# Kernel tuning notes

Hardware: AMD Instinct MI355X
Metric: run time of the kernel (lower is better)

## Reference

```python
import jax, jax.numpy as jnp
import numpy as np

EPS = 1e-5
NEG = 0.1  # LeakyReLU slope


def _conv(x, w, stride=1, pad=0):
    return jax.lax.conv_general_dilated(
        x, w, (stride, stride), [(pad, pad), (pad, pad)],
        dimension_numbers=('NCHW', 'OIHW', 'NCHW'))


def _bn(x, p):
    # p: [4, C] stacked (gamma, beta, running_mean, running_var); eval-mode BN
    g, b, m, v = p[0], p[1], p[2], p[3]
    inv = g / jnp.sqrt(v + EPS)
    return x * inv[None, :, None, None] + (b - m * inv)[None, :, None, None]


def _lrelu(x):
    return jnp.where(x >= 0, x, NEG * x)


def _mdcn(x, w_off, b_off, w_dcn, b_dcn, G=2, K=3, pad=1):
    # ModulatedDeformConvPack (DCNv2): conv_offset -> (dy, dx, mask), then
    # modulated bilinear sampling + dense contraction with the conv weight.
    B, C, H, W = x.shape
    K2 = K * K
    off = _conv(x, w_off, 1, pad) + b_off[None, :, None, None]  # [B, 3*G*K2, H, W]
    dy, dx, ml = jnp.split(off, 3, axis=1)
    dy = dy.reshape(B, G, K2, H, W)
    dx = dx.reshape(B, G, K2, H, W)
    mask = jax.nn.sigmoid(ml).reshape(B, G, K2, H, W)
    kyv, kxv = np.meshgrid(np.arange(K), np.arange(K), indexing='ij')
    ky = jnp.asarray(kyv.reshape(K2), x.dtype)
    kx = jnp.asarray(kxv.reshape(K2), x.dtype)
    ii = jnp.arange(H, dtype=x.dtype)
    jj = jnp.arange(W, dtype=x.dtype)
    # sample coords: p0 + p_k + offset (stride 1, dilation 1)
    py = ii[None, None, None, :, None] - pad + ky[None, None, :, None, None] + dy
    px = jj[None, None, None, None, :] - pad + kx[None, None, :, None, None] + dx
    Cg = C // G
    # [B, G, H*W, Cg] layout so the bilinear gather indexes a small int tensor
    imgs = x.reshape(B, G, Cg, H, W).transpose(0, 1, 3, 4, 2).reshape(B, G, H * W, Cg)
    y0 = jnp.floor(py)
    x0 = jnp.floor(px)
    N = K2 * H * W
    wy = (py - y0).reshape(B, G, N, 1)
    wx = (px - x0).reshape(B, G, N, 1)

    def gather(yi, xi):
        valid = (yi >= 0) & (yi <= H - 1) & (xi >= 0) & (xi <= W - 1)
        yc = jnp.clip(yi, 0, H - 1).astype(jnp.int32)
        xc = jnp.clip(xi, 0, W - 1).astype(jnp.int32)
        idx = (yc * W + xc).reshape(B, G, N, 1)
        v = jnp.take_along_axis(imgs, idx, axis=2)  # [B, G, N, Cg]
        return v * valid.reshape(B, G, N, 1).astype(x.dtype)

    v00 = gather(y0, x0)
    v01 = gather(y0, x0 + 1)
    v10 = gather(y0 + 1, x0)
    v11 = gather(y0 + 1, x0 + 1)
    val = (v00 * (1 - wy) * (1 - wx) + v01 * (1 - wy) * wx
           + v10 * wy * (1 - wx) + v11 * wy * wx)
    val = (val * mask.reshape(B, G, N, 1)).reshape(B, G, K2, H, W, Cg)
    wr = w_dcn.reshape(w_dcn.shape[0], G, Cg, K2)
    out = jnp.einsum('bgkijc,ogck->boij', val, wr)
    return out + b_dcn[None, :, None, None]


def _forward(x, w_r1, bn_r1, w_r2, bn_r2, w_rs, bn_rs, w_off, b_off,
             w_dcn, b_dcn, bn1, w_c2, bn2, w_ds, bn_ds):
    # ResBlock(in=64, out=128, stride=2): conv3x3/s2-BN-LReLU-conv3x3-BN + 1x1/s2 shortcut
    h = _lrelu(_bn(_conv(x, w_r1, 2, 1), bn_r1))
    h = _bn(_conv(h, w_r2, 1, 1), bn_r2)
    sc = _bn(_conv(x, w_rs, 2, 0), bn_rs)
    h = _lrelu(h + sc)
    # modulated deformable conv 3x3, deformable_groups=2
    h = _lrelu(_bn(_mdcn(h, w_off, b_off, w_dcn, b_dcn), bn1))
    h = _lrelu(_bn(_conv(h, w_c2, 1, 0), bn2))
    # DeconBlock residual (downsample since in!=out, stride!=1)
    res = _bn(_conv(x, w_ds, 2, 0), bn_ds)
    return res + h


def setup_inputs() -> dict:
    key = jax.random.key(0)
    ks = jax.random.split(key, 16)
    f32 = jnp.float32

    def n(k, shape, s):
        return jax.random.normal(k, shape, f32) * s

    def bnp(k, c):
        # gamma, beta, mean, var — var kept >= 0.1 for stability
        return jax.random.uniform(k, (4, c), f32, 0.1, 1.0)

    return {
        'x': n(ks[0], (4, 64, 192, 192), 1.0),
        'w_r1': n(ks[1], (128, 64, 3, 3), 0.04),
        'bn_r1': bnp(ks[2], 128),
        'w_r2': n(ks[3], (128, 128, 3, 3), 0.03),
        'bn_r2': bnp(ks[4], 128),
        'w_rs': n(ks[5], (128, 64, 1, 1), 0.12),
        'bn_rs': bnp(ks[6], 128),
        'w_off': n(ks[7], (54, 128, 3, 3), 0.01),  # small => offsets of a few px
        'b_off': n(ks[8], (54,), 0.1),
        'w_dcn': n(ks[9], (128, 128, 3, 3), 0.03),
        'b_dcn': n(ks[10], (128,), 0.1),
        'bn1': bnp(ks[11], 128),
        'w_c2': n(ks[12], (128, 128, 1, 1), 0.09),
        'bn2': bnp(ks[13], 128),
        'w_ds': n(ks[14], (128, 64, 1, 1), 0.12),
        'bn_ds': bnp(ks[15], 128),
    }


def reference(x, w_r1, bn_r1, w_r2, bn_r2, w_rs, bn_rs, w_off, b_off,
              w_dcn, b_dcn, bn1, w_c2, bn2, w_ds, bn_ds):
    return _forward(x, w_r1, bn_r1, w_r2, bn_r2, w_rs, bn_rs, w_off, b_off,
                    w_dcn, b_dcn, bn1, w_c2, bn2, w_ds, bn_ds)
```

## Files before the change

kernel.cpp:

```cpp
#include <hip/hip_runtime.h>
#include <hip/hip_bf16.h>
#include <cstdint>

#define EPS 1e-5f
#define NEG 0.1f

using bfrag = __attribute__((ext_vector_type(8))) short;
using f32x4 = __attribute__((ext_vector_type(4))) float;
typedef unsigned short ushort_t;

constexpr int B_  = 4,  CIN = 64, H0 = 192, W0 = 192;
constexpr int C_  = 128, H_ = 96, W_ = 96;
constexpr int HW_ = H_ * W_;
constexpr int HW0 = H0 * W0;
constexpr int XS  = 194;
constexpr int TS  = 98;
constexpr int VSTR = 1160;

__device__ __forceinline__ ushort_t f2bf(float f) {
  unsigned u = __builtin_bit_cast(unsigned, f);
  u += 0x7fffu + ((u >> 16) & 1u);
  return (ushort_t)(u >> 16);
}
__device__ __forceinline__ float loF(unsigned d) {
  return __builtin_bit_cast(float, d << 16);
}
__device__ __forceinline__ float hiF(unsigned d) {
  return __builtin_bit_cast(float, d & 0xFFFF0000u);
}
__device__ __forceinline__ bfrag loadB(const ushort_t* p) {
  return *(const bfrag*)p;
}

#define MFMA4(A0, A1, B0, B1, ACC)                                             \
  ACC[0][0] = __builtin_amdgcn_mfma_f32_16x16x32_bf16(A0, B0, ACC[0][0], 0, 0, 0); \
  ACC[0][1] = __builtin_amdgcn_mfma_f32_16x16x32_bf16(A0, B1, ACC[0][1], 0, 0, 0); \
  ACC[1][0] = __builtin_amdgcn_mfma_f32_16x16x32_bf16(A1, B0, ACC[1][0], 0, 0, 0); \
  ACC[1][1] = __builtin_amdgcn_mfma_f32_16x16x32_bf16(A1, B1, ACC[1][1], 0, 0, 0);

__global__ __launch_bounds__(256)
void k_prep(const float* __restrict__ x,
            const float* __restrict__ w_r1, const float* __restrict__ w_r2,
            const float* __restrict__ w_off, const float* __restrict__ w_dcn,
            const float* __restrict__ w_rs, const float* __restrict__ w_c2,
            const float* __restrict__ w_ds,
            ushort_t* __restrict__ wp_r1, ushort_t* __restrict__ wp_r2,
            ushort_t* __restrict__ wp_off, ushort_t* __restrict__ wp_dcn,
            ushort_t* __restrict__ wp_rs, ushort_t* __restrict__ wp_c2,
            ushort_t* __restrict__ wp_ds,
            ushort_t* __restrict__ xclp, ushort_t* __restrict__ t1p,
            ushort_t* __restrict__ t3p) {
  __shared__ float tile[64][65];
  int bi = blockIdx.x;
  int tid = (int)threadIdx.x;
  auto pack3w = [&](const float* w, ushort_t* wp, int O, int C, int Opad, int b0) {
    int idx = (bi - b0) * 256 + tid;
    int e = idx & 7;
    int lane = (idx >> 3) & 63;
    int fb = idx >> 9;
    int OBQ = Opad / 16;
    int obq = fb % OBQ, s = fb / OBQ;
    int lr = lane & 15, lq = lane >> 4;
    int o = obq * 16 + lr;
    int cq = s % (C / 32), tap = s / (C / 32);
    int c = cq * 32 + lq * 8 + e;
    wp[idx] = (o < O) ? f2bf(w[((size_t)o * C + c) * 9 + tap]) : (ushort_t)0;
  };
  auto pack1w = [&](const float* w, ushort_t* wp, int O, int C, int Opad, int b0) {
    int idx = (bi - b0) * 256 + tid;
    int e = idx & 7;
    int lane = (idx >> 3) & 63;
    int fb = idx >> 9;
    int OBQ = Opad / 16;
    int obq = fb % OBQ, s = fb / OBQ;
    int lr = lane & 15, lq = lane >> 4;
    int o = obq * 16 + lr;
    int c = s * 32 + lq * 8 + e;
    wp[idx] = (o < O) ? f2bf(w[(size_t)o * C + c]) : (ushort_t)0;
  };
  auto border = [&](ushort_t* buf, int N, int C, int b0) {
    int idx = (bi - b0) * 256 + tid;
    int per = 4 * N - 4;
    if (idx >= per * 4) return;
    int b = idx / per, e = idx - b * per;
    int r, s;
    if (e < N) { r = 0; s = e; }
    else if (e < 2 * N) { r = N - 1; s = e - N; }
    else if (e < 3 * N - 2) { r = e - 2 * N + 1; s = 0; }
    else { r = e - (3 * N - 2) + 1; s = N - 1; }
    uint4* p = (uint4*)(buf + ((size_t)(b * N + r) * N + s) * C);
#pragma unroll
    for (int t = 0; t < 16; ++t) { if (t < C / 8) p[t] = make_uint4(0, 0, 0, 0); }
  };
  if      (bi <  288) pack3w(w_r1,  wp_r1, 128,  64, 128, 0);
  else if (bi <  864) pack3w(w_r2,  wp_r2, 128, 128, 128, 288);
  else if (bi < 1152) pack3w(w_off, wp_off, 54, 128,  64, 864);
  else if (bi < 1728) pack3w(w_dcn, wp_dcn, 128, 128, 128, 1152);
  else if (bi < 1760) pack1w(w_rs,  wp_rs, 128,  64, 128, 1728);
  else if (bi < 1824) pack1w(w_c2,  wp_c2, 128, 128, 128, 1760);
  else if (bi < 1856) pack1w(w_ds,  wp_ds, 128,  64, 128, 1824);
  else if (bi < 1869) border(xclp, XS, 64, 1856);
  else if (bi < 1876) border(t1p, TS, 128, 1869);
  else if (bi < 1883) border(t3p, TS, 128, 1876);
  else {
    int bx = bi - 1883;
    int cx = bx % 3;
    int rem = bx / 3;
    int y = rem % 192, b = rem / 192;
    int tx = tid & 63, ty = tid >> 6;
    const float* src = x + (size_t)b * CIN * HW0 + (size_t)y * W0 + cx * 64;
#pragma unroll
    for (int r = 0; r < 16; ++r) {
      int ch = r * 4 + ty;
      tile[ch][tx] = src[(size_t)ch * HW0 + tx];
    }
    __syncthreads();
    ushort_t* dst = xclp + ((size_t)(b * XS + y + 1) * XS + cx * 64 + 1) * 64;
#pragma unroll
    for (int r = 0; r < 16; ++r) {
      int pp = r * 4 + ty;
      dst[(size_t)pp * 64 + tx] = f2bf(tile[tx][pp]);
    }
  }
}

__global__ __launch_bounds__(256)
void k_conv1(const ushort_t* __restrict__ xclp, const ushort_t* __restrict__ wp,
             const float* __restrict__ bnp, ushort_t* __restrict__ t1p) {
  __shared__ ushort_t at[5 * 66 * 64];
  int tid = threadIdx.x, lane = tid & 63, wv = tid >> 6;
  int lr = lane & 15, lq = lane >> 4, ob = wv * 32;
  int j0 = blockIdx.x * 32, i0 = blockIdx.y * 2, b = blockIdx.z;
  for (int t = tid; t < 2640; t += 256) {
    int ky = t / 528, r = t - ky * 528;
    int p = r >> 3, c8 = r & 7;
    const char* src = (const char*)(xclp +
        ((size_t)(b * XS + 2 * i0 + ky) * XS + 2 * j0) * 64) + p * 128 + c8 * 16;
    int db = ((ky * 66 + p) * 128 + c8 * 16) ^ (((p >> 1) & 7) << 4);
    *(uint4*)((char*)at + db) = *(const uint4*)src;
  }
  __syncthreads();
  f32x4 acc[2][2][2] = {};
#pragma unroll
  for (int tap = 0; tap < 9; ++tap) {
    int ky = tap / 3, kx = tap - 3 * ky;
    int pxa = 2 * lr + kx, pxb = 2 * (16 + lr) + kx;
#pragma unroll
    for (int cq = 0; cq < 2; ++cq) {
      int s = tap * 2 + cq;
      bfrag b0 = loadB(wp + (size_t)(s * 8 + wv * 2) * 512 + lane * 8);
      bfrag b1 = loadB(wp + (size_t)(s * 8 + wv * 2 + 1) * 512 + lane * 8);
#pragma unroll
      for (int r = 0; r < 2; ++r) {
        int kr = 2 * r + ky;
        bfrag a0 = *(const bfrag*)((const char*)at +
            (((kr * 66 + pxa) * 128 + cq * 64 + lq * 16) ^ (((pxa >> 1) & 7) << 4)));
        bfrag a1 = *(const bfrag*)((const char*)at +
            (((kr * 66 + pxb) * 128 + cq * 64 + lq * 16) ^ (((pxb >> 1) & 7) << 4)));
        MFMA4(a0, a1, b0, b1, acc[r]);
      }
    }
  }
#pragma unroll
  for (int r = 0; r < 2; ++r) {
    ushort_t* dst = t1p + ((size_t)(b * TS + i0 + r + 1) * TS + j0 + 1) * 128;
#pragma unroll
    for (int nf = 0; nf < 2; ++nf) {
      int o = ob + nf * 16 + lr;
      float inv = bnp[o] * rsqrtf(bnp[384 + o] + EPS);
      float bb = bnp[128 + o] - bnp[256 + o] * inv;
#pragma unroll
      for (int mf = 0; mf < 2; ++mf)
#pragma unroll
        for (int jj = 0; jj < 4; ++jj) {
          int pix = mf * 16 + 4 * lq + jj;
          float v = acc[r][mf][nf][jj] * inv + bb;
          v = v >= 0.f ? v : NEG * v;
          dst[(size_t)pix * 128 + o] = f2bf(v);
        }
    }
  }
}

__global__ __launch_bounds__(256)
void k_conv2(const ushort_t* __restrict__ t1p, const ushort_t* __restrict__ xclp,
             const ushort_t* __restrict__ wp2, const ushort_t* __restrict__ wprs,
             const float* __restrict__ bn2p, const float* __restrict__ bnsp,
             ushort_t* __restrict__ t3p) {
  __shared__ ushort_t at[4 * 34 * 128];
  int tid = threadIdx.x, lane = tid & 63, wv = tid >> 6;
  int lr = lane & 15, lq = lane >> 4, ob = wv * 32;
  int j0 = blockIdx.x * 32, i0 = blockIdx.y * 2, b = blockIdx.z;
  for (int t = tid; t < 2176; t += 256) {
    int ky = t / 544, r = t - ky * 544;
    int p = r >> 4, c16 = r & 15;
    const char* src = (const char*)(t1p +
        ((size_t)(b * TS + i0 + ky) * TS + j0) * 128) + p * 256 + c16 * 16;
    int db = ((ky * 34 + p) * 256 + c16 * 16) ^ ((p & 7) << 4);
    *(uint4*)((char*)at + db) = *(const uint4*)src;
  }
  __syncthreads();
  f32x4 acc[2][2][2] = {};
  f32x4 acs[2][2][2] = {};
#pragma unroll
  for (int tap = 0; tap < 9; ++tap) {
    int ky = tap / 3, kx = tap - 3 * ky;
    int pxa = lr + kx, pxb = 16 + lr + kx;
#pragma unroll
    for (int cq = 0; cq < 4; ++cq) {
      int s = tap * 4 + cq;
      bfrag b0 = loadB(wp2 + (size_t)(s * 8 + wv * 2) * 512 + lane * 8);
      bfrag b1 = loadB(wp2 + (size_t)(s * 8 + wv * 2 + 1) * 512 + lane * 8);
#pragma unroll
      for (int r = 0; r < 2; ++r) {
        int kr = r + ky;
        bfrag a0 = *(const bfrag*)((const char*)at +
            (((kr * 34 + pxa) * 256 + cq * 64 + lq * 16) ^ ((pxa & 7) << 4)));
        bfrag a1 = *(const bfrag*)((const char*)at +
            (((kr * 34 + pxb) * 256 + cq * 64 + lq * 16) ^ ((pxb & 7) << 4)));
        MFMA4(a0, a1, b0, b1, acc[r]);
      }
    }
  }
#pragma unroll
  for (int r = 0; r < 2; ++r) {
    const ushort_t* rowp = xclp + (size_t)(b * XS + 2 * (i0 + r) + 1) * XS * 64;
    const ushort_t* pa = rowp + (size_t)(2 * (j0 + lr) + 1) * 64 + 8 * lq;
    const ushort_t* pb = rowp + (size_t)(2 * (j0 + 16 + lr) + 1) * 64 + 8 * lq;
#pragma unroll
    for (int sq = 0; sq < 2; ++sq) {
      bfrag a0 = loadB(pa + sq * 32);
      bfrag a1 = loadB(pb + sq * 32);
      bfrag b0 = loadB(wprs + (size_t)(sq * 8 + wv * 2) * 512 + lane * 8);
      bfrag b1 = loadB(wprs + (size_t)(sq * 8 + wv * 2 + 1) * 512 + lane * 8);
      MFMA4(a0, a1, b0, b1, acs[r]);
    }
  }
#pragma unroll
  for (int r = 0; r < 2; ++r) {
    ushort_t* dst = t3p + ((size_t)(b * TS + i0 + r + 1) * TS + j0 + 1) * 128;
#pragma unroll
    for (int nf = 0; nf < 2; ++nf) {
      int o = ob + nf * 16 + lr;
      float i2 = bn2p[o] * rsqrtf(bn2p[384 + o] + EPS);
      float b2 = bn2p[128 + o] - bn2p[256 + o] * i2;
      float is = bnsp[o] * rsqrtf(bnsp[384 + o] + EPS);
      float bs = bnsp[128 + o] - bnsp[256 + o] * is;
#pragma unroll
      for (int mf = 0; mf < 2; ++mf)
#pragma unroll
        for (int jj = 0; jj < 4; ++jj) {
          int pix = mf * 16 + 4 * lq + jj;
          float h = acc[r][mf][nf][jj] * i2 + b2 + acs[r][mf][nf][jj] * is + bs;
          h = h >= 0.f ? h : NEG * h;
          dst[(size_t)pix * 128 + o] = f2bf(h);
        }
    }
  }
}

__global__ __launch_bounds__(512)
void k_dcn(const ushort_t* __restrict__ t3p, const ushort_t* __restrict__ wpo,
           const float* __restrict__ boff, const ushort_t* __restrict__ wp,
           const float* __restrict__ bdcn, const float* __restrict__ bnp,
           ushort_t* __restrict__ t4cl) {
  __shared__ ushort_t val[16 * VSTR];
  __shared__ float offb_lds[16 * 64];
  int tid = threadIdx.x;
  int j0 = blockIdx.x * 16, i = blockIdx.y, b = blockIdx.z;
  int lane = tid & 63, wv = tid >> 6;
  int lr = lane & 15, lq = lane >> 4;

  {
    char* at = (char*)val;
    for (int t = tid; t < 864; t += 512) {
      int ky = t / 288, r = t - ky * 288;
      int p = r >> 4, c16b = r & 15;
      const char* src = (const char*)(t3p +
          ((size_t)(b * TS + i + ky) * TS + j0 + p) * 128) + c16b * 16;
      int db = ((ky * 18 + p) * 256 + c16b * 16) ^ ((p & 7) << 4);
      *(uint4*)(at + db) = *(const uint4*)src;
    }
    __syncthreads();
    int ot = wv & 3, kh = wv >> 2;
    f32x4 pacc = {};
#pragma unroll
    for (int s9 = 0; s9 < 18; ++s9) {
      int s = kh * 18 + s9;
      int tap = s >> 2, cq = s & 3;
      int ky = tap / 3, kx = tap - 3 * ky;
      int px = lr + kx;
      bfrag a0 = *(const bfrag*)(at +
          (((ky * 18 + px) * 256 + cq * 64 + lq * 16) ^ ((px & 7) << 4)));
      bfrag b0 = loadB(wpo + (size_t)(s * 4 + ot) * 512 + lane * 8);
      pacc = __builtin_amdgcn_mfma_f32_16x16x32_bf16(a0, b0, pacc, 0, 0, 0);
    }
    float* red = (float*)((char*)val + 16384);
    if (kh == 1) {
      *(f32x4*)(red + ot * 256 + lane * 4) = pacc;
    }
    __syncthreads();
    if (kh == 0) {
      f32x4 v = *(const f32x4*)(red + ot * 256 + lane * 4);
      pacc += v;
      int o = ot * 16 + lr;
      float bias = (o < 54) ? boff[o] : 0.f;
#pragma unroll
      for (int jj = 0; jj < 4; ++jj) {
        int px = 4 * lq + jj;
        offb_lds[px * 64 + o] = pacc[jj] + bias;
      }
    }
    __syncthreads();
  }

  int gq = tid >> 4;
  int c16 = tid & 15;
  int pix = gq >> 1, g = gq & 1;
  int gl = (gq & 3) * 16;
  int my_b = 0; unsigned my_w0 = 0, my_w1 = 0;
  if (c16 < 9) {
    int k = c16, gk = g * 9 + k;
    int ky = k / 3, kx = k - 3 * ky;
    int j = j0 + pix;
    const float* ob_ = offb_lds + pix * 64;
    float dy = ob_[gk];
    float dx = ob_[18 + gk];
    float ml = ob_[36 + gk];
    float mk = 1.f / (1.f + __expf(-ml));
    float py = (float)(i - 1 + ky) + dy;
    float px = (float)(j - 1 + kx) + dx;
    float fy = floorf(py), fx = floorf(px);
    float wy = py - fy, wx = px - fx;
    int y0 = (int)fy, x0 = (int)fx;
    bool yv0 = (unsigned)y0 < 96u, yv1 = (unsigned)(y0 + 1) < 96u;
    bool xv0 = (unsigned)x0 < 96u, xv1 = (unsigned)(x0 + 1) < 96u;
    float w00 = (yv0 && xv0) ? (1.f - wy) * (1.f - wx) * mk : 0.f;
    float w01 = (yv0 && xv1) ? (1.f - wy) * wx * mk : 0.f;
    float w10 = (yv1 && xv0) ? wy * (1.f - wx) * mk : 0.f;
    float w11 = (yv1 && xv1) ? wy * wx * mk : 0.f;
    int yb = min(max(y0, -1), 95), xb = min(max(x0, -1), 95);
    my_b = (((yb + 1) * TS + xb + 1) * 128 + g * 64) * 2;
    my_w0 = (unsigned)f2bf(w00) | ((unsigned)f2bf(w01) << 16);
    my_w1 = (unsigned)f2bf(w10) | ((unsigned)f2bf(w11) << 16);
  }
  __syncthreads();

  const char* imgb = (const char*)(t3p + (size_t)b * TS * TS * 128) + c16 * 8;
  char* vrow = (char*)val + pix * (VSTR * 2) + g * 128 + c16 * 8;
#pragma unroll
  for (int k = 0; k < 9; ++k) {
    int gb = __shfl(my_b, gl + k, 64);
    unsigned w0 = (unsigned)__shfl((int)my_w0, gl + k, 64);
    unsigned w1 = (unsigned)__shfl((int)my_w1, gl + k, 64);
    const char* pA = imgb + gb;
    uint2 d00 = *(const uint2*)pA;
    uint2 d01 = *(const uint2*)(pA + 256);
    uint2 d10 = *(const uint2*)(pA + TS * 256);
    uint2 d11 = *(const uint2*)(pA + TS * 256 + 256);
    float w00 = loF(w0), w01 = hiF(w0);
    float w10 = loF(w1), w11 = hiF(w1);
    unsigned o2[2];
#pragma unroll
    for (int t = 0; t < 2; ++t) {
      unsigned e00 = ((const unsigned*)&d00)[t];
      unsigned e01 = ((const unsigned*)&d01)[t];
      unsigned e10 = ((const unsigned*)&d10)[t];
      unsigned e11 = ((const unsigned*)&d11)[t];
      float slo = loF(e00) * w00 + loF(e01) * w01 + loF(e10) * w10 + loF(e11) * w11;
      float shi = hiF(e00) * w00 + hiF(e01) * w01 + hiF(e10) * w10 + hiF(e11) * w11;
      unsigned u0 = __builtin_bit_cast(unsigned, slo) + 0x8000u;
      unsigned u1 = __builtin_bit_cast(unsigned, shi) + 0x8000u;
      o2[t] = __builtin_amdgcn_perm(u1, u0, 0x07060302u);
    }
    *(uint2*)(vrow + k * 256) = make_uint2(o2[0], o2[1]);
  }
  __syncthreads();

  int ob = wv * 16;
  f32x4 acc = {};
  for (int s = 0; s < 36; ++s) {
    bfrag a0 = *(const bfrag*)&val[lr * VSTR + 32 * s + 8 * lq];
    bfrag b0 = loadB(wp + (size_t)(s * 8 + wv) * 512 + lane * 8);
    acc = __builtin_amdgcn_mfma_f32_16x16x32_bf16(a0, b0, acc, 0, 0, 0);
  }

  {
    ushort_t* dst = t4cl + ((size_t)(b * 96 + i) * 96 + j0) * 128;
    int o = ob + lr;
    float inv = bnp[o] * rsqrtf(bnp[384 + o] + EPS);
    float bb = bnp[128 + o] - bnp[256 + o] * inv;
    float bd = bdcn[o];
#pragma unroll
    for (int jj = 0; jj < 4; ++jj) {
      int pixw = 4 * lq + jj;
      float r = (acc[jj] + bd) * inv + bb;
      r = r >= 0.f ? r : NEG * r;
      dst[(size_t)pixw * 128 + o] = f2bf(r);
    }
  }
}

__global__ __launch_bounds__(256)
void k_final(const ushort_t* __restrict__ t4cl, const ushort_t* __restrict__ xclp,
             const ushort_t* __restrict__ wpc2, const ushort_t* __restrict__ wpds,
             const float* __restrict__ bn2p, const float* __restrict__ bndsp,
             float* __restrict__ outp) {
  __shared__ float ol[128 * 36];
  int tid = threadIdx.x, lane = tid & 63, wv = tid >> 6;
  int lr = lane & 15, lq = lane >> 4, ob = wv * 32;
  int j0 = blockIdx.x * 32, i = blockIdx.y, b = blockIdx.z;
  f32x4 acc[2][2] = {};
  f32x4 acs[2][2] = {};
  {
    const ushort_t* rowp = t4cl + ((size_t)(b * 96 + i) * 96 + j0) * 128;
#pragma unroll
    for (int s = 0; s < 4; ++s) {
      bfrag a0 = loadB(rowp + (size_t)lr * 128 + s * 32 + 8 * lq);
      bfrag a1 = loadB(rowp + (size_t)(16 + lr) * 128 + s * 32 + 8 * lq);
      bfrag b0 = loadB(wpc2 + (size_t)(s * 8 + wv * 2) * 512 + lane * 8);
      bfrag b1 = loadB(wpc2 + (size_t)(s * 8 + wv * 2 + 1) * 512 + lane * 8);
      MFMA4(a0, a1, b0, b1, acc);
    }
  }
  {
    const ushort_t* rowx = xclp + (size_t)(b * XS + 2 * i + 1) * XS * 64;
    const ushort_t* pa = rowx + (size_t)(2 * (j0 + lr) + 1) * 64 + 8 * lq;
    const ushort_t* pb = rowx + (size_t)(2 * (j0 + 16 + lr) + 1) * 64 + 8 * lq;
#pragma unroll
    for (int s = 0; s < 2; ++s) {
      bfrag a0 = loadB(pa + s * 32);
      bfrag a1 = loadB(pb + s * 32);
      bfrag b0 = loadB(wpds + (size_t)(s * 8 + wv * 2) * 512 + lane * 8);
      bfrag b1 = loadB(wpds + (size_t)(s * 8 + wv * 2 + 1) * 512 + lane * 8);
      MFMA4(a0, a1, b0, b1, acs);
    }
  }
#pragma unroll
  for (int nf = 0; nf < 2; ++nf) {
    int o = ob + nf * 16 + lr;
    float i2 = bn2p[o] * rsqrtf(bn2p[384 + o] + EPS);
    float b2 = bn2p[128 + o] - bn2p[256 + o] * i2;
    float id = bndsp[o] * rsqrtf(bndsp[384 + o] + EPS);
    float bd = bndsp[128 + o] - bndsp[256 + o] * id;
#pragma unroll
    for (int mf = 0; mf < 2; ++mf)
#pragma unroll
      for (int jj = 0; jj < 4; ++jj) {
        int pix = mf * 16 + 4 * lq + jj;
        float h = acc[mf][nf][jj] * i2 + b2;
        h = h >= 0.f ? h : NEG * h;
        float res = acs[mf][nf][jj] * id + bd;
        ol[o * 36 + pix] = res + h;
      }
  }
  __syncthreads();
#pragma unroll
  for (int r = 0; r < 4; ++r) {
    int idx = r * 256 + tid;
    int o = idx >> 3, p4 = idx & 7;
    f32x4 v = *(const f32x4*)&ol[o * 36 + p4 * 4];
    *(f32x4*)&outp[((size_t)(b * C_ + o) * H_ + i) * W_ + j0 + p4 * 4] = v;
  }
}

extern "C" void kernel_launch(void* const* d_in, const int* in_sizes, int n_in,
                              void* d_out, int out_size, void* d_ws, size_t ws_size,
                              hipStream_t stream) {
  const float* x     = (const float*)d_in[0];
  const float* w_r1  = (const float*)d_in[1];
  const float* bn_r1 = (const float*)d_in[2];
  const float* w_r2  = (const float*)d_in[3];
  const float* bn_r2 = (const float*)d_in[4];
  const float* w_rs  = (const float*)d_in[5];
  const float* bn_rs = (const float*)d_in[6];
  const float* w_off = (const float*)d_in[7];
  const float* b_off = (const float*)d_in[8];
  const float* w_dcn = (const float*)d_in[9];
  const float* b_dcn = (const float*)d_in[10];
  const float* bn1   = (const float*)d_in[11];
  const float* w_c2  = (const float*)d_in[12];
  const float* bn2   = (const float*)d_in[13];
  const float* w_ds  = (const float*)d_in[14];
  const float* bn_ds = (const float*)d_in[15];
  float* out = (float*)d_out;

  ushort_t* base  = (ushort_t*)d_ws;
  ushort_t* xclp  = base;
  ushort_t* t1p   = base + 9634816;
  ushort_t* t3p   = base + 14552064;
  ushort_t* wp_r1 = base + 19469312;
  ushort_t* wp_r2 = wp_r1 + 73728;
  ushort_t* wp_off= wp_r2 + 147456;
  ushort_t* wp_dcn= wp_off + 73728;
  ushort_t* wp_rs = wp_dcn + 147456;
  ushort_t* wp_c2 = wp_rs + 8192;
  ushort_t* wp_ds = wp_c2 + 16384;
  ushort_t* t4cl  = t1p;

  k_prep<<<4187, 256, 0, stream>>>(x, w_r1, w_r2, w_off, w_dcn, w_rs, w_c2,
                                   w_ds, wp_r1, wp_r2, wp_off, wp_dcn, wp_rs,
                                   wp_c2, wp_ds, xclp, t1p, t3p);

  k_conv1<<<dim3(3, 48, 4), 256, 0, stream>>>(xclp, wp_r1, bn_r1, t1p);
  k_conv2<<<dim3(3, 48, 4), 256, 0, stream>>>(t1p, xclp, wp_r2, wp_rs, bn_r2, bn_rs, t3p);
  k_dcn  <<<dim3(6, 96, 4), 512, 0, stream>>>(t3p, wp_off, b_off, wp_dcn, b_dcn, bn1, t4cl);
  k_final<<<dim3(3, 96, 4), 256, 0, stream>>>(t4cl, xclp, wp_c2, wp_ds, bn2, bn_ds, out);
}
```

Before: 127.0 us.

## Widen DCN tile to 32 pixels and chunk sampling/MFMA over tap groups

Each DCN block now handles 32 output pixels instead of 16, halving the grid, so each weight fragment loaded for the main contraction feeds two MFMAs. The offset conv splits waves by pixel half instead of by K-halves, which removes the cross-wave reduction and its barrier. The bilinear sampling is split into three chunks of three taps each, interleaved with the MFMA contraction, to keep the sampled-value LDS buffer small. This adds extra barriers and halves block-level parallelism.

```diff
diff --git a/kernel.cpp b/kernel.cpp
--- a/kernel.cpp
+++ b/kernel.cpp
@@ -15,7 +15,7 @@
 constexpr int HW0 = H0 * W0;
 constexpr int XS  = 194;
 constexpr int TS  = 98;
-constexpr int VSTR = 1160;
+constexpr int VROW = 392;
 
 __device__ __forceinline__ ushort_t f2bf(float f) {
   unsigned u = __builtin_bit_cast(unsigned, f);
@@ -264,125 +264,132 @@
            const float* __restrict__ boff, const ushort_t* __restrict__ wp,
            const float* __restrict__ bdcn, const float* __restrict__ bnp,
            ushort_t* __restrict__ t4cl) {
-  __shared__ ushort_t val[16 * VSTR];
-  __shared__ float offb_lds[16 * 64];
+  __shared__ char smem[26112];
+  __shared__ float offb_lds[32 * 64];
   int tid = threadIdx.x;
-  int j0 = blockIdx.x * 16, i = blockIdx.y, b = blockIdx.z;
+  int j0 = blockIdx.x * 32, i = blockIdx.y, b = blockIdx.z;
   int lane = tid & 63, wv = tid >> 6;
   int lr = lane & 15, lq = lane >> 4;
 
   {
-    char* at = (char*)val;
-    for (int t = tid; t < 864; t += 512) {
-      int ky = t / 288, r = t - ky * 288;
+    for (int t = tid; t < 1632; t += 512) {
+      int ky = t / 544, r = t - ky * 544;
       int p = r >> 4, c16b = r & 15;
       const char* src = (const char*)(t3p +
           ((size_t)(b * TS + i + ky) * TS + j0 + p) * 128) + c16b * 16;
-      int db = ((ky * 18 + p) * 256 + c16b * 16) ^ ((p & 7) << 4);
-      *(uint4*)(at + db) = *(const uint4*)src;
+      int db = ((ky * 34 + p) * 256 + c16b * 16) ^ ((p & 7) << 4);
+      *(uint4*)(smem + db) = *(const uint4*)src;
     }
     __syncthreads();
-    int ot = wv & 3, kh = wv >> 2;
+    int ot = wv >> 1, half = wv & 1;
     f32x4 pacc = {};
 #pragma unroll
-    for (int s9 = 0; s9 < 18; ++s9) {
-      int s = kh * 18 + s9;
+    for (int s = 0; s < 36; ++s) {
       int tap = s >> 2, cq = s & 3;
       int ky = tap / 3, kx = tap - 3 * ky;
-      int px = lr + kx;
-      bfrag a0 = *(const bfrag*)(at +
-          (((ky * 18 + px) * 256 + cq * 64 + lq * 16) ^ ((px & 7) << 4)));
+      int px = half * 16 + lr + kx;
+      bfrag a0 = *(const bfrag*)(smem +
+          (((ky * 34 + px) * 256 + cq * 64 + lq * 16) ^ ((px & 7) << 4)));
       bfrag b0 = loadB(wpo + (size_t)(s * 4 + ot) * 512 + lane * 8);
       pacc = __builtin_amdgcn_mfma_f32_16x16x32_bf16(a0, b0, pacc, 0, 0, 0);
     }
-    float* red = (float*)((char*)val + 16384);
-    if (kh == 1) {
-      *(f32x4*)(red + ot * 256 + lane * 4) = pacc;
-    }
-    __syncthreads();
-    if (kh == 0) {
-      f32x4 v = *(const f32x4*)(red + ot * 256 + lane * 4);
-      pacc += v;
-      int o = ot * 16 + lr;
-      float bias = (o < 54) ? boff[o] : 0.f;
-#pragma unroll
-      for (int jj = 0; jj < 4; ++jj) {
-        int px = 4 * lq + jj;
-        offb_lds[px * 64 + o] = pacc[jj] + bias;
-      }
+    int o = ot * 16 + lr;
+    float bias = (o < 54) ? boff[o] : 0.f;
+#pragma unroll
+    for (int jj = 0; jj < 4; ++jj) {
+      int px = half * 16 + 4 * lq + jj;
+      offb_lds[px * 64 + o] = pacc[jj] + bias;
     }
     __syncthreads();
   }
 
   int gq = tid >> 4;
   int c16 = tid & 15;
-  int pix = gq >> 1, g = gq & 1;
   int gl = (gq & 3) * 16;
-  int my_b = 0; unsigned my_w0 = 0, my_w1 = 0;
+  int my_b0 = 0, my_b1 = 0;
+  unsigned my_w00 = 0, my_w10 = 0, my_w01 = 0, my_w11 = 0;
   if (c16 < 9) {
-    int k = c16, gk = g * 9 + k;
+    int k = c16;
     int ky = k / 3, kx = k - 3 * ky;
-    int j = j0 + pix;
-    const float* ob_ = offb_lds + pix * 64;
-    float dy = ob_[gk];
-    float dx = ob_[18 + gk];
-    float ml = ob_[36 + gk];
-    float mk = 1.f / (1.f + __expf(-ml));
-    float py = (float)(i - 1 + ky) + dy;
-    float px = (float)(j - 1 + kx) + dx;
-    float fy = floorf(py), fx = floorf(px);
-    float wy = py - fy, wx = px - fx;
-    int y0 = (int)fy, x0 = (int)fx;
-    bool yv0 = (unsigned)y0 < 96u, yv1 = (unsigned)(y0 + 1) < 96u;
-    bool xv0 = (unsigned)x0 < 96u, xv1 = (unsigned)(x0 + 1) < 96u;
-    float w00 = (yv0 && xv0) ? (1.f - wy) * (1.f - wx) * mk : 0.f;
-    float w01 = (yv0 && xv1) ? (1.f - wy) * wx * mk : 0.f;
-    float w10 = (yv1 && xv0) ? wy * (1.f - wx) * mk : 0.f;
-    float w11 = (yv1 && xv1) ? wy * wx * mk : 0.f;
-    int yb = min(max(y0, -1), 95), xb = min(max(x0, -1), 95);
-    my_b = (((yb + 1) * TS + xb + 1) * 128 + g * 64) * 2;
-    my_w0 = (unsigned)f2bf(w00) | ((unsigned)f2bf(w01) << 16);
-    my_w1 = (unsigned)f2bf(w10) | ((unsigned)f2bf(w11) << 16);
+    int j = j0 + gq;
+    const float* ob_ = offb_lds + gq * 64;
+#pragma unroll
+    for (int g = 0; g < 2; ++g) {
+      int gk = g * 9 + k;
+      float dy = ob_[gk];
+      float dx = ob_[18 + gk];
+      float ml = ob_[36 + gk];
+      float mk = 1.f / (1.f + __expf(-ml));
+      float py = (float)(i - 1 + ky) + dy;
+      float px = (float)(j - 1 + kx) + dx;
+      float fy = floorf(py), fx = floorf(px);
+      float wy = py - fy, wx = px - fx;
+      int y0 = (int)fy, x0 = (int)fx;
+      bool yv0 = (unsigned)y0 < 96u, yv1 = (unsigned)(y0 + 1) < 96u;
+      bool xv0 = (unsigned)x0 < 96u, xv1 = (unsigned)(x0 + 1) < 96u;
+      float w00 = (yv0 && xv0) ? (1.f - wy) * (1.f - wx) * mk : 0.f;
+      float w01 = (yv0 && xv1) ? (1.f - wy) * wx * mk : 0.f;
+      float w10 = (yv1 && xv0) ? wy * (1.f - wx) * mk : 0.f;
+      float w11 = (yv1 && xv1) ? wy * wx * mk : 0.f;
+      int yb = min(max(y0, -1), 95), xb = min(max(x0, -1), 95);
+      int bb = (((yb + 1) * TS + xb + 1) * 128 + g * 64) * 2;
+      unsigned pw0 = (unsigned)f2bf(w00) | ((unsigned)f2bf(w01) << 16);
+      unsigned pw1 = (unsigned)f2bf(w10) | ((unsigned)f2bf(w11) << 16);
+      if (g == 0) { my_b0 = bb; my_w00 = pw0; my_w10 = pw1; }
+      else        { my_b1 = bb; my_w01 = pw0; my_w11 = pw1; }
+    }
   }
   __syncthreads();
 
+  ushort_t* val = (ushort_t*)smem;
   const char* imgb = (const char*)(t3p + (size_t)b * TS * TS * 128) + c16 * 8;
-  char* vrow = (char*)val + pix * (VSTR * 2) + g * 128 + c16 * 8;
-#pragma unroll
-  for (int k = 0; k < 9; ++k) {
-    int gb = __shfl(my_b, gl + k, 64);
-    unsigned w0 = (unsigned)__shfl((int)my_w0, gl + k, 64);
-    unsigned w1 = (unsigned)__shfl((int)my_w1, gl + k, 64);
-    const char* pA = imgb + gb;
-    uint2 d00 = *(const uint2*)pA;
-    uint2 d01 = *(const uint2*)(pA + 256);
-    uint2 d10 = *(const uint2*)(pA + TS * 256);
-    uint2 d11 = *(const uint2*)(pA + TS * 256 + 256);
-    float w00 = loF(w0), w01 = hiF(w0);
-    float w10 = loF(w1), w11 = hiF(w1);
-    unsigned o2[2];
-#pragma unroll
-    for (int t = 0; t < 2; ++t) {
-      unsigned e00 = ((const unsigned*)&d00)[t];
-      unsigned e01 = ((const unsigned*)&d01)[t];
-      unsigned e10 = ((const unsigned*)&d10)[t];
-      unsigned e11 = ((const unsigned*)&d11)[t];
-      float slo = loF(e00) * w00 + loF(e01) * w01 + loF(e10) * w10 + loF(e11) * w11;
-      float shi = hiF(e00) * w00 + hiF(e01) * w01 + hiF(e10) * w10 + hiF(e11) * w11;
-      unsigned u0 = __builtin_bit_cast(unsigned, slo) + 0x8000u;
-      unsigned u1 = __builtin_bit_cast(unsigned, shi) + 0x8000u;
-      o2[t] = __builtin_amdgcn_perm(u1, u0, 0x07060302u);
-    }
-    *(uint2*)(vrow + k * 256) = make_uint2(o2[0], o2[1]);
-  }
-  __syncthreads();
-
+  char* vrow = (char*)val + gq * (VROW * 2) + c16 * 8;
   int ob = wv * 16;
-  f32x4 acc = {};
-  for (int s = 0; s < 36; ++s) {
-    bfrag a0 = *(const bfrag*)&val[lr * VSTR + 32 * s + 8 * lq];
-    bfrag b0 = loadB(wp + (size_t)(s * 8 + wv) * 512 + lane * 8);
-    acc = __builtin_amdgcn_mfma_f32_16x16x32_bf16(a0, b0, acc, 0, 0, 0);
+  f32x4 acc0 = {}, acc1 = {};
+#pragma unroll
+  for (int c = 0; c < 3; ++c) {
+#pragma unroll
+    for (int g = 0; g < 2; ++g) {
+#pragma unroll
+      for (int kc = 0; kc < 3; ++kc) {
+        int k = 3 * c + kc;
+        int gb = __shfl(g == 0 ? my_b0 : my_b1, gl + k, 64);
+        unsigned w0 = (unsigned)__shfl((int)(g == 0 ? my_w00 : my_w01), gl + k, 64);
+        unsigned w1 = (unsigned)__shfl((int)(g == 0 ? my_w10 : my_w11), gl + k, 64);
+        const char* pA = imgb + gb;
+        uint2 d00 = *(const uint2*)pA;
+        uint2 d01 = *(const uint2*)(pA + 256);
+        uint2 d10 = *(const uint2*)(pA + TS * 256);
+        uint2 d11 = *(const uint2*)(pA + TS * 256 + 256);
+        float w00 = loF(w0), w01 = hiF(w0);
+        float w10 = loF(w1), w11 = hiF(w1);
+        unsigned o2[2];
+#pragma unroll
+        for (int t = 0; t < 2; ++t) {
+          unsigned e00 = ((const unsigned*)&d00)[t];
+          unsigned e01 = ((const unsigned*)&d01)[t];
+          unsigned e10 = ((const unsigned*)&d10)[t];
+          unsigned e11 = ((const unsigned*)&d11)[t];
+          float slo = loF(e00) * w00 + loF(e01) * w01 + loF(e10) * w10 + loF(e11) * w11;
+          float shi = hiF(e00) * w00 + hiF(e01) * w01 + hiF(e10) * w10 + hiF(e11) * w11;
+          unsigned u0 = __builtin_bit_cast(unsigned, slo) + 0x8000u;
+          unsigned u1 = __builtin_bit_cast(unsigned, shi) + 0x8000u;
+          o2[t] = __builtin_amdgcn_perm(u1, u0, 0x07060302u);
+        }
+        *(uint2*)(vrow + kc * 256 + g * 128) = make_uint2(o2[0], o2[1]);
+      }
+    }
+    __syncthreads();
+#pragma unroll
+    for (int sl = 0; sl < 12; ++sl) {
+      int s = c * 12 + sl;
+      bfrag a0 = *(const bfrag*)&val[lr * VROW + 32 * sl + 8 * lq];
+      bfrag a1 = *(const bfrag*)&val[(16 + lr) * VROW + 32 * sl + 8 * lq];
+      bfrag b0 = loadB(wp + (size_t)(s * 8 + wv) * 512 + lane * 8);
+      acc0 = __builtin_amdgcn_mfma_f32_16x16x32_bf16(a0, b0, acc0, 0, 0, 0);
+      acc1 = __builtin_amdgcn_mfma_f32_16x16x32_bf16(a1, b0, acc1, 0, 0, 0);
+    }
+    if (c < 2) __syncthreads();
   }
 
   {
@@ -393,10 +400,13 @@
     float bd = bdcn[o];
 #pragma unroll
     for (int jj = 0; jj < 4; ++jj) {
-      int pixw = 4 * lq + jj;
-      float r = (acc[jj] + bd) * inv + bb;
-      r = r >= 0.f ? r : NEG * r;
-      dst[(size_t)pixw * 128 + o] = f2bf(r);
+      int p0 = 4 * lq + jj;
+      float r0 = (acc0[jj] + bd) * inv + bb;
+      r0 = r0 >= 0.f ? r0 : NEG * r0;
+      dst[(size_t)p0 * 128 + o] = f2bf(r0);
+      float r1 = (acc1[jj] + bd) * inv + bb;
+      r1 = r1 >= 0.f ? r1 : NEG * r1;
+      dst[(size_t)(16 + p0) * 128 + o] = f2bf(r1);
     }
   }
 }
@@ -504,6 +514,6 @@
 
   k_conv1<<<dim3(3, 48, 4), 256, 0, stream>>>(xclp, wp_r1, bn_r1, t1p);
   k_conv2<<<dim3(3, 48, 4), 256, 0, stream>>>(t1p, xclp, wp_r2, wp_rs, bn_r2, bn_rs, t3p);
-  k_dcn  <<<dim3(6, 96, 4), 512, 0, stream>>>(t3p, wp_off, b_off, wp_dcn, b_dcn, bn1, t4cl);
+  k_dcn  <<<dim3(3, 96, 4), 512, 0, stream>>>(t3p, wp_off, b_off, wp_dcn, b_dcn, bn1, t4cl);
   k_final<<<dim3(3, 96, 4), 256, 0, stream>>>(t4cl, xclp, wp_c2, wp_ds, bn2, bn_ds, out);
 }
```

New measurement: 121.7 us. -4.1%, faster.
